# Optimization experiments

Hardware: AMD Instinct MI355X
Metric: run time of the kernel (lower is better)

The kernel has to match this reference:

```python
import jax, jax.numpy as jnp
import numpy as np

B, L, ENC, EMB, H, V = 64, 33, 512, 256, 512, 32000


def setup_inputs() -> dict:
    key = jax.random.key(0)
    ks = jax.random.split(key, 16)
    x = jax.random.normal(ks[0], (B, ENC), dtype=jnp.float32)
    padded_target = jax.random.randint(ks[1], (B, L), 0, V)
    target_lengths = jax.random.randint(ks[2], (B,), 2, L + 1)
    target_lengths = target_lengths.at[0].set(L)  # pin max length -> static step count
    s = 0.05
    return {
        "x": x,
        "padded_target": padded_target,
        "target_lengths": target_lengths,
        "embed": jax.random.normal(ks[3], (V, EMB), dtype=jnp.float32) * s,
        "W_h0": jax.random.normal(ks[4], (H, ENC), dtype=jnp.float32) * s,
        "b_h0": jnp.zeros((H,), jnp.float32),
        "W_c0": jax.random.normal(ks[5], (H, ENC), dtype=jnp.float32) * s,
        "b_c0": jnp.zeros((H,), jnp.float32),
        "W_ih": jax.random.normal(ks[6], (4 * H, ENC + EMB), dtype=jnp.float32) * s,
        "W_hh": jax.random.normal(ks[7], (4 * H, H), dtype=jnp.float32) * s,
        "b_ih": jnp.zeros((4 * H,), jnp.float32),
        "b_hh": jnp.zeros((4 * H,), jnp.float32),
        "W_out": jax.random.normal(ks[8], (V, H), dtype=jnp.float32) * s,
        "b_out": jnp.zeros((V,), jnp.float32),
    }


def reference(x, padded_target, target_lengths, embed, W_h0, b_h0, W_c0, b_c0,
              W_ih, W_hh, b_ih, b_hh, W_out, b_out):
    # sort by length, descending (packed-sequence ordering)
    sorted_indices = jnp.argsort(-target_lengths)
    x = x[sorted_indices]                      # [B, ENC]
    tgt = padded_target[sorted_indices]        # [B, L]
    lens = target_lengths[sorted_indices] - 1  # decode steps per row
    emb = embed[tgt]                           # [B, L, EMB]

    h = x @ W_h0.T + b_h0                      # context-initialized state
    c = x @ W_c0.T + b_c0
    T = padded_target.shape[1] - 1             # static max steps (max len pinned to L)

    def step(carry, inp):
        h, c = carry
        e_t, t = inp
        active = (lens > t)[:, None]           # rows still decoding (prefix, sorted)
        g = jnp.concatenate([x, e_t], axis=1) @ W_ih.T + b_ih + h @ W_hh.T + b_hh
        i, f, gg, o = jnp.split(g, 4, axis=1)  # torch LSTMCell gate order i,f,g,o
        c_new = jax.nn.sigmoid(f) * c + jax.nn.sigmoid(i) * jnp.tanh(gg)
        h_new = jax.nn.sigmoid(o) * jnp.tanh(c_new)
        h = jnp.where(active, h_new, h)        # inactive rows keep frozen state
        c = jnp.where(active, c_new, c)
        pred = jnp.where(active, h_new @ W_out.T + b_out, 0.0)  # dropout p=0
        return (h, c), pred

    (_, _), preds = jax.lax.scan(
        step, (h, c), (jnp.transpose(emb[:, :T], (1, 0, 2)), jnp.arange(T)))
    prediction = jnp.transpose(preds, (1, 0, 2))  # [B, T, V]
    return prediction, sorted_indices
```

## Files before the change

kernel.cpp:

```cpp
#include <hip/hip_runtime.h>

typedef __attribute__((ext_vector_type(8))) short short8;
typedef __attribute__((ext_vector_type(8))) unsigned short ushort8;
typedef __attribute__((ext_vector_type(4))) float f32x4;

#define DEV __device__ __forceinline__

DEV unsigned short f2bf(float f) {
  unsigned int u = __float_as_uint(f);
  u += 0x7fffu + ((u >> 16) & 1u);
  return (unsigned short)(u >> 16);
}
DEV float sigm(float x) { return 1.f / (1.f + __expf(-x)); }
DEV float tanh_(float x) { return 1.f - 2.f / (1.f + __expf(2.f * x)); }

typedef __attribute__((address_space(1))) const void* as1cv;
typedef __attribute__((address_space(3))) void* as3v;
DEV void gll16(const void* g, void* l) {
  __builtin_amdgcn_global_load_lds((as1cv)g, (as3v)l, 16, 0, 0);
}

__global__ void __launch_bounds__(256) k_sort(const float* __restrict__ x,
    const int* __restrict__ ptar, const int* __restrict__ tlen,
    int* __restrict__ sidx, int* __restrict__ lens, int* __restrict__ base,
    int* __restrict__ inv, int* __restrict__ Pw, int* __restrict__ tok,
    float* __restrict__ xs, float* __restrict__ tail) {
  __shared__ int ss[64], ls[64], bs[64];
  int tid = threadIdx.x;
  if (tid < 64) {
    int li = tlen[tid];
    int rank = 0;
    for (int j = 0; j < 64; ++j) {
      int lj = tlen[j];
      rank += (lj > li || (lj == li && j < tid)) ? 1 : 0;
    }
    ss[rank] = tid;
  }
  __syncthreads();
  if (tid < 64) {
    int src = ss[tid];
    sidx[tid] = src;
    int l = tlen[src] - 1;
    ls[tid] = l;
    lens[tid] = l;
    tail[tid] = (float)src;
  }
  __syncthreads();
  if (tid == 0) {
    int s = 0;
    for (int b = 0; b < 64; ++b) { bs[b] = s; base[b] = s; s += ls[b]; }
    Pw[0] = s;
  }
  __syncthreads();
  for (int idx = tid; idx < 2048; idx += 256) {
    int b = idx >> 5, t = idx & 31;
    if (t < ls[b]) inv[bs[b] + t] = idx;
  }
  for (int idx = tid; idx < 32 * 64; idx += 256) {
    int t = idx >> 6, b = idx & 63;
    tok[idx] = ptar[ss[b] * 33 + t];
  }
  for (int idx = tid; idx < 64 * 512; idx += 256) {
    int b = idx >> 9;
    xs[idx] = x[ss[b] * 512 + (idx & 511)];
  }
}

__global__ void __launch_bounds__(256) k_convmany(
    const float* __restrict__ W_h0, const float* __restrict__ W_c0,
    const float* __restrict__ W_ih, const float* __restrict__ W_hh,
    const float* __restrict__ xs,
    unsigned short* __restrict__ Wpro, unsigned short* __restrict__ Wihb2,
    unsigned short* __restrict__ Whb, unsigned short* __restrict__ xsb) {
  long long g = (long long)(blockIdx.x * 256 + threadIdx.x) * 8;
  const float* src;
  unsigned short* dst;
  if (g < 262144) {
    src = W_h0 + g; dst = Wpro + g;
  } else if (g < 524288) {
    long long l = g - 262144; src = W_c0 + l; dst = Wpro + 262144 + l;
  } else if (g < 1572864) {
    long long l = g - 524288;
    long long r = l >> 9, c = l & 511;
    src = W_ih + r * 768 + c; dst = Wpro + 524288 + l;
  } else if (g < 2097152) {
    long long l = g - 1572864;
    long long r = l >> 8, c = l & 255;
    src = W_ih + r * 768 + 512 + c; dst = Wihb2 + l;
  } else if (g < 3145728) {
    long long l = g - 2097152; src = W_hh + l; dst = Whb + l;
  } else {
    long long l = g - 3145728; src = xs + l; dst = xsb + l;
  }
  float4 v0 = *(const float4*)src, v1 = *(const float4*)(src + 4);
  ushort8 o;
  o[0] = f2bf(v0.x); o[1] = f2bf(v0.y); o[2] = f2bf(v0.z); o[3] = f2bf(v0.w);
  o[4] = f2bf(v1.x); o[5] = f2bf(v1.y); o[6] = f2bf(v1.z); o[7] = f2bf(v1.w);
  *(ushort8*)dst = o;
}

__global__ void __launch_bounds__(256) k_pro(const unsigned short* __restrict__ xsb,
    const unsigned short* __restrict__ Wpro, const float* __restrict__ b_h0,
    const float* __restrict__ b_c0, const float* __restrict__ b_ih,
    const float* __restrict__ b_hh, unsigned short* __restrict__ h0b,
    float* __restrict__ c, float* __restrict__ gx) {
  int tid = threadIdx.x, lane = tid & 63, w = tid >> 6;
  int n0 = blockIdx.x * 64 + w * 16;
  int lr = lane & 15, lk = lane >> 4;
  f32x4 acc[4];
#pragma unroll
  for (int i = 0; i < 4; ++i) acc[i] = (f32x4){0.f, 0.f, 0.f, 0.f};
  const unsigned short* B = Wpro + (size_t)(n0 + lr) * 512 + lk * 8;
  const unsigned short* A = xsb + (size_t)lr * 512 + lk * 8;
#pragma unroll
  for (int ks = 0; ks < 16; ++ks) {
    short8 bfr = *(const short8*)(B + ks * 32);
#pragma unroll
    for (int mi = 0; mi < 4; ++mi) {
      short8 af = *(const short8*)(A + mi * 16 * 512 + ks * 32);
      acc[mi] = __builtin_amdgcn_mfma_f32_16x16x32_bf16(af, bfr, acc[mi], 0, 0, 0);
    }
  }
  int n = n0 + lr;
#pragma unroll
  for (int mi = 0; mi < 4; ++mi)
#pragma unroll
    for (int r = 0; r < 4; ++r) {
      int b = mi * 16 + lk * 4 + r;
      float v = acc[mi][r];
      if (n < 512) {
        h0b[b * 512 + n] = f2bf(v + b_h0[n]);
      } else if (n < 1024) {
        int u = n - 512;
        c[b * 512 + u] = v + b_c0[u];
      } else {
        int j = n - 1024;
        gx[(size_t)b * 2048 + j] = v + b_ih[j] + b_hh[j];
      }
    }
}

__global__ void __launch_bounds__(256) k_emb(const int* __restrict__ tok,
    const float* __restrict__ embed, unsigned short* __restrict__ Eb) {
  int gid = blockIdx.x * 256 + threadIdx.x;
  int row = gid >> 5, c8 = (gid & 31) * 8;
  const float* src = embed + (size_t)tok[row] * 256 + c8;
  float4 v0 = *(const float4*)src, v1 = *(const float4*)(src + 4);
  ushort8 o;
  o[0] = f2bf(v0.x); o[1] = f2bf(v0.y); o[2] = f2bf(v0.z); o[3] = f2bf(v0.w);
  o[4] = f2bf(v1.x); o[5] = f2bf(v1.y); o[6] = f2bf(v1.z); o[7] = f2bf(v1.w);
  *(ushort8*)(Eb + (size_t)row * 256 + c8) = o;
}

__global__ void __launch_bounds__(256) k_ga2(const unsigned short* __restrict__ Eb,
    const unsigned short* __restrict__ Wb2, const float* __restrict__ gx,
    float* __restrict__ GA, const float* __restrict__ W_out,
    unsigned short* __restrict__ Wob) {
  int bid = blockIdx.x;
  int tid = threadIdx.x;
  if (bid >= 256) {
    long long basei = (long long)(bid - 256) * 65536;
#pragma unroll 4
    for (int it = 0; it < 32; ++it) {
      long long i = basei + (long long)it * 2048 + tid * 8;
      float4 v0 = *(const float4*)(W_out + i);
      float4 v1 = *(const float4*)(W_out + i + 4);
      ushort8 o;
      o[0] = f2bf(v0.x); o[1] = f2bf(v0.y); o[2] = f2bf(v0.z); o[3] = f2bf(v0.w);
      o[4] = f2bf(v1.x); o[5] = f2bf(v1.y); o[6] = f2bf(v1.z); o[7] = f2bf(v1.w);
      *(ushort8*)(Wob + i) = o;
    }
    return;
  }
  __shared__ alignas(16) char ldsbuf[32768];
  char* ldsA = ldsbuf;
  char* ldsB = ldsbuf + 16384;
  int mt = bid & 15, nt = bid >> 4;
  int m0 = mt * 128, n0 = nt * 128;
  int lane = tid & 63, w = tid >> 6;
  int wm = w >> 1, wn = w & 1;
  f32x4 acc[4][4];
#pragma unroll
  for (int a = 0; a < 4; ++a)
#pragma unroll
    for (int bq = 0; bq < 4; ++bq) acc[a][bq] = (f32x4){0.f, 0.f, 0.f, 0.f};
  const unsigned short* Arow = Eb + (size_t)m0 * 256;
  const unsigned short* Brow = Wb2 + (size_t)n0 * 256;
  for (int kt = 0; kt < 4; ++kt) {
    int k0 = kt * 64;
    if (kt) __syncthreads();
#pragma unroll
    for (int j = 0; j < 4; ++j) {
      int ci = j * 256 + w * 64 + lane;
      int r = ci >> 3;
      int clog = ((ci & 7) << 4) ^ ((r & 7) << 4);
      int ldst = (j * 256 + w * 64) * 16;
      gll16((const char*)(Arow + (size_t)r * 256 + k0) + clog, ldsA + ldst);
      gll16((const char*)(Brow + (size_t)r * 256 + k0) + clog, ldsB + ldst);
    }
    __syncthreads();
#pragma unroll
    for (int kk = 0; kk < 2; ++kk) {
      short8 af[4], bf[4];
      int cb = kk * 64 + (lane >> 4) * 16;
#pragma unroll
      for (int i = 0; i < 4; ++i) {
        int ar = wm * 64 + i * 16 + (lane & 15);
        af[i] = *(const short8*)(ldsA + ar * 128 + (cb ^ ((ar & 7) << 4)));
        int br = wn * 64 + i * 16 + (lane & 15);
        bf[i] = *(const short8*)(ldsB + br * 128 + (cb ^ ((br & 7) << 4)));
      }
#pragma unroll
      for (int mi = 0; mi < 4; ++mi)
#pragma unroll
        for (int ni = 0; ni < 4; ++ni)
          acc[mi][ni] = __builtin_amdgcn_mfma_f32_16x16x32_bf16(
              af[mi], bf[ni], acc[mi][ni], 0, 0, 0);
    }
  }
#pragma unroll
  for (int mi = 0; mi < 4; ++mi) {
    int mb = m0 + wm * 64 + mi * 16 + ((lane >> 4) << 2);
#pragma unroll
    for (int r = 0; r < 4; ++r) {
      int m = mb + r;
#pragma unroll
      for (int ni = 0; ni < 4; ++ni) {
        int j = n0 + wn * 64 + ni * 16 + (lane & 15);
        GA[(size_t)m * 2048 + j] = acc[mi][ni][r] + gx[(size_t)(m & 63) * 2048 + j];
      }
    }
  }
}

__global__ void __launch_bounds__(256) k_step3(
    const unsigned short* __restrict__ hin, unsigned short* __restrict__ hout,
    float* __restrict__ c, const float* __restrict__ GA,
    const unsigned short* __restrict__ Whb, const int* __restrict__ lens,
    const int* __restrict__ base, unsigned short* __restrict__ Hm, int t) {
  __shared__ float Gs[4][16][16];
  int tid = threadIdx.x, lane = tid & 63, g = tid >> 6;
  int lr = lane & 15, lk = lane >> 4;
  int mq = blockIdx.x & 3, ug = blockIdx.x >> 2;
  int r0 = mq * 16, u0 = ug * 16;

  const float* gab = GA + ((size_t)t * 64 + r0) * 2048 + g * 512 + u0 + lr;
  float gv[4];
#pragma unroll
  for (int r = 0; r < 4; ++r) gv[r] = gab[(size_t)(lk * 4 + r) * 2048];

  const unsigned short* Bp = Whb + (size_t)(g * 512 + u0 + lr) * 512 + lk * 8;
  const unsigned short* Ap = hin + (size_t)(r0 + lr) * 512 + lk * 8;
  f32x4 acc = (f32x4){0.f, 0.f, 0.f, 0.f};
#pragma unroll
  for (int ks = 0; ks < 16; ++ks) {
    short8 a0 = *(const short8*)(Ap + ks * 32);
    short8 b0 = *(const short8*)(Bp + ks * 32);
    acc = __builtin_amdgcn_mfma_f32_16x16x32_bf16(a0, b0, acc, 0, 0, 0);
  }
#pragma unroll
  for (int r = 0; r < 4; ++r) Gs[g][lk * 4 + r][lr] = acc[r] + gv[r];
  __syncthreads();

  int row = tid >> 4, uc = tid & 15;
  int b = r0 + row, u = u0 + uc;
  float fi = Gs[0][row][uc], ff = Gs[1][row][uc];
  float fg = Gs[2][row][uc], fo = Gs[3][row][uc];
  float cold = c[b * 512 + u];
  float cn = sigm(ff) * cold + sigm(fi) * tanh_(fg);
  float hn = sigm(fo) * tanh_(cn);
  bool act = lens[b] > t;
  if (act) c[b * 512 + u] = cn;
  unsigned short hbv = f2bf(hn);
  hout[b * 512 + u] = act ? hbv : hin[b * 512 + u];
  if (act) Hm[((size_t)(base[b] + t)) * 512 + u] = hbv;
}

__global__ void __launch_bounds__(256) k_zf(const int* __restrict__ lens,
    float* __restrict__ out) {
  int m = blockIdx.x;
  int b = m >> 5, t = m & 31;
  if (lens[b] > t) return;
  float4 z = {0.f, 0.f, 0.f, 0.f};
  float* row = out + (size_t)m * 32000;
  for (int i = threadIdx.x * 4; i < 32000; i += 1024)
    *(float4*)(row + i) = z;
}

__global__ void __launch_bounds__(512) k_gemm(const unsigned short* __restrict__ Hm,
    const unsigned short* __restrict__ Wb, const float* __restrict__ b_out,
    const int* __restrict__ inv, const int* __restrict__ Pw,
    float* __restrict__ out) {
  __shared__ alignas(16) char ldsbuf[49152];
  char* ldsA = ldsbuf;
  char* ldsB = ldsbuf + 16384;
  int P = Pw[0];
  int sb = (blockIdx.x & 7) * 250 + (blockIdx.x >> 3);
  int mt = sb % 16, nt = sb / 16;
  int m0 = mt * 128, n0 = nt * 256;
  if (m0 >= P) return;
  int tid = threadIdx.x, lane = tid & 63, w = tid >> 6;
  int wm = w >> 2, wn = w & 3;
  f32x4 acc[4][4];
#pragma unroll
  for (int a = 0; a < 4; ++a)
#pragma unroll
    for (int bq = 0; bq < 4; ++bq) acc[a][bq] = (f32x4){0.f, 0.f, 0.f, 0.f};
  const unsigned short* Arow = Hm + (size_t)m0 * 512;
  const unsigned short* Brow = Wb + (size_t)n0 * 512;
  for (int kt = 0; kt < 8; ++kt) {
    int k0 = kt * 64;
    if (kt) __syncthreads();
#pragma unroll
    for (int j = 0; j < 2; ++j) {
      int ci = j * 512 + tid;
      int r = ci >> 3;
      int clog = ((ci & 7) << 4) ^ ((r & 7) << 4);
      gll16((const char*)(Arow + (size_t)r * 512 + k0) + clog, ldsA + ci * 16);
    }
#pragma unroll
    for (int j = 0; j < 4; ++j) {
      int ci = j * 512 + tid;
      int r = ci >> 3;
      int clog = ((ci & 7) << 4) ^ ((r & 7) << 4);
      gll16((const char*)(Brow + (size_t)r * 512 + k0) + clog, ldsB + ci * 16);
    }
    __syncthreads();
#pragma unroll
    for (int kk = 0; kk < 2; ++kk) {
      short8 af[4], bf[4];
      int cb = kk * 64 + (lane >> 4) * 16;
#pragma unroll
      for (int i = 0; i < 4; ++i) {
        int ar = wm * 64 + i * 16 + (lane & 15);
        af[i] = *(const short8*)(ldsA + ar * 128 + (cb ^ ((ar & 7) << 4)));
        int br = wn * 64 + i * 16 + (lane & 15);
        bf[i] = *(const short8*)(ldsB + br * 128 + (cb ^ ((br & 7) << 4)));
      }
#pragma unroll
      for (int mi = 0; mi < 4; ++mi)
#pragma unroll
        for (int ni = 0; ni < 4; ++ni)
          acc[mi][ni] = __builtin_amdgcn_mfma_f32_16x16x32_bf16(
              af[mi], bf[ni], acc[mi][ni], 0, 0, 0);
    }
  }
#pragma unroll
  for (int mi = 0; mi < 4; ++mi) {
    int pb = m0 + wm * 64 + mi * 16 + ((lane >> 4) << 2);
#pragma unroll
    for (int r = 0; r < 4; ++r) {
      int p = pb + r;
      if (p >= P) continue;
      size_t orow = (size_t)inv[p] * 32000;
#pragma unroll
      for (int ni = 0; ni < 4; ++ni) {
        int n = n0 + wn * 64 + ni * 16 + (lane & 15);
        out[orow + n] = acc[mi][ni][r] + b_out[n];
      }
    }
  }
}

extern "C" void kernel_launch(void* const* d_in, const int* in_sizes, int n_in,
                              void* d_out, int out_size, void* d_ws, size_t ws_size,
                              hipStream_t stream) {
  const float* x     = (const float*)d_in[0];
  const int*   ptar  = (const int*)d_in[1];
  const int*   tlen  = (const int*)d_in[2];
  const float* embed = (const float*)d_in[3];
  const float* W_h0  = (const float*)d_in[4];
  const float* b_h0  = (const float*)d_in[5];
  const float* W_c0  = (const float*)d_in[6];
  const float* b_c0  = (const float*)d_in[7];
  const float* W_ih  = (const float*)d_in[8];
  const float* W_hh  = (const float*)d_in[9];
  const float* b_ih  = (const float*)d_in[10];
  const float* b_hh  = (const float*)d_in[11];
  const float* W_out = (const float*)d_in[12];
  const float* b_out = (const float*)d_in[13];
  float* out = (float*)d_out;

  char* ws = (char*)d_ws;
  size_t off = 0;
  auto alloc = [&](size_t bytes) {
    void* p = ws + off;
    off += (bytes + 255) & ~(size_t)255;
    return p;
  };
  unsigned short* Wob = (unsigned short*)alloc(32000ull * 512 * 2);
  unsigned short* Hm  = (unsigned short*)alloc(2048ull * 512 * 2);
  float* xs   = (float*)alloc(64 * 512 * 4);
  unsigned short* h0b = (unsigned short*)alloc(64 * 512 * 2);
  unsigned short* h1b = (unsigned short*)alloc(64 * 512 * 2);
  float* cbuf = (float*)alloc(64 * 512 * 4);
  float* gx   = (float*)alloc(64 * 2048 * 4);
  int* sidx = (int*)alloc(64 * 4);
  int* lens = (int*)alloc(64 * 4);
  int* base = (int*)alloc(64 * 4);
  int* inv  = (int*)alloc(2048 * 4);
  int* Pw   = (int*)alloc(4);
  int* tok  = (int*)alloc(2048 * 4);

  float* GA = out;
  unsigned short* Wpro  = (unsigned short*)(out + 4194304);
  unsigned short* Wihb2 = (unsigned short*)(out + 4980736);
  unsigned short* Whb   = (unsigned short*)(out + 5242880);
  unsigned short* Eb    = (unsigned short*)(out + 5767168);
  unsigned short* xsb   = (unsigned short*)(out + 6029312);
  float* tail = out + 65536000;

  k_sort<<<1, 256, 0, stream>>>(x, ptar, tlen, sidx, lens, base, inv, Pw, tok,
                                xs, tail);
  k_convmany<<<1552, 256, 0, stream>>>(W_h0, W_c0, W_ih, W_hh, xs,
                                       Wpro, Wihb2, Whb, xsb);
  k_pro<<<48, 256, 0, stream>>>(xsb, Wpro, b_h0, b_c0, b_ih, b_hh, h0b, cbuf, gx);
  k_emb<<<256, 256, 0, stream>>>(tok, embed, Eb);
  k_ga2<<<506, 256, 0, stream>>>(Eb, Wihb2, gx, GA, W_out, Wob);

  unsigned short* hb[2] = {h0b, h1b};
  for (int t = 0; t < 32; ++t)
    k_step3<<<128, 256, 0, stream>>>(hb[t & 1], hb[(t + 1) & 1], cbuf, GA, Whb,
                                     lens, base, Hm, t);

  k_zf<<<2048, 256, 0, stream>>>(lens, out);
  k_gemm<<<2000, 512, 0, stream>>>(Hm, Wob, b_out, inv, Pw, out);
  (void)in_sizes; (void)n_in; (void)out_size; (void)ws_size;
}
```

Measured before the change: 362.4 us.

## Fuse prep kernels and overlap W_out conversion with recurrent steps

```diff
diff --git a/kernel.cpp b/kernel.cpp
--- a/kernel.cpp
+++ b/kernel.cpp
@@ -20,13 +20,43 @@
   __builtin_amdgcn_global_load_lds((as1cv)g, (as3v)l, 16, 0, 0);
 }
 
-__global__ void __launch_bounds__(256) k_sort(const float* __restrict__ x,
+__global__ void __launch_bounds__(256) k_pre(const float* __restrict__ x,
     const int* __restrict__ ptar, const int* __restrict__ tlen,
+    const float* __restrict__ W_h0, const float* __restrict__ W_c0,
+    const float* __restrict__ W_ih, const float* __restrict__ W_hh,
     int* __restrict__ sidx, int* __restrict__ lens, int* __restrict__ base,
     int* __restrict__ inv, int* __restrict__ Pw, int* __restrict__ tok,
-    float* __restrict__ xs, float* __restrict__ tail) {
+    unsigned short* __restrict__ xsb, float* __restrict__ tail,
+    unsigned short* __restrict__ Wpro, unsigned short* __restrict__ Wihb2,
+    unsigned short* __restrict__ Whb) {
+  int bid = blockIdx.x, tid = threadIdx.x;
+  if (bid > 0) {
+    long long g = (long long)(bid - 1) * 2048 + tid * 8;
+    const float* src;
+    unsigned short* dst;
+    if (g < 262144) {
+      src = W_h0 + g; dst = Wpro + g;
+    } else if (g < 524288) {
+      long long l = g - 262144; src = W_c0 + l; dst = Wpro + 262144 + l;
+    } else if (g < 1572864) {
+      long long l = g - 524288;
+      long long r = l >> 9, c = l & 511;
+      src = W_ih + r * 768 + c; dst = Wpro + 524288 + l;
+    } else if (g < 2097152) {
+      long long l = g - 1572864;
+      long long r = l >> 8, c = l & 255;
+      src = W_ih + r * 768 + 512 + c; dst = Wihb2 + l;
+    } else {
+      long long l = g - 2097152; src = W_hh + l; dst = Whb + l;
+    }
+    float4 v0 = *(const float4*)src, v1 = *(const float4*)(src + 4);
+    ushort8 o;
+    o[0] = f2bf(v0.x); o[1] = f2bf(v0.y); o[2] = f2bf(v0.z); o[3] = f2bf(v0.w);
+    o[4] = f2bf(v1.x); o[5] = f2bf(v1.y); o[6] = f2bf(v1.z); o[7] = f2bf(v1.w);
+    *(ushort8*)dst = o;
+    return;
+  }
   __shared__ int ss[64], ls[64], bs[64];
-  int tid = threadIdx.x;
   if (tid < 64) {
     int li = tlen[tid];
     int rank = 0;
@@ -62,50 +92,31 @@
   }
   for (int idx = tid; idx < 64 * 512; idx += 256) {
     int b = idx >> 9;
-    xs[idx] = x[ss[b] * 512 + (idx & 511)];
-  }
-}
-
-__global__ void __launch_bounds__(256) k_convmany(
-    const float* __restrict__ W_h0, const float* __restrict__ W_c0,
-    const float* __restrict__ W_ih, const float* __restrict__ W_hh,
-    const float* __restrict__ xs,
-    unsigned short* __restrict__ Wpro, unsigned short* __restrict__ Wihb2,
-    unsigned short* __restrict__ Whb, unsigned short* __restrict__ xsb) {
-  long long g = (long long)(blockIdx.x * 256 + threadIdx.x) * 8;
-  const float* src;
-  unsigned short* dst;
-  if (g < 262144) {
-    src = W_h0 + g; dst = Wpro + g;
-  } else if (g < 524288) {
-    long long l = g - 262144; src = W_c0 + l; dst = Wpro + 262144 + l;
-  } else if (g < 1572864) {
-    long long l = g - 524288;
-    long long r = l >> 9, c = l & 511;
-    src = W_ih + r * 768 + c; dst = Wpro + 524288 + l;
-  } else if (g < 2097152) {
-    long long l = g - 1572864;
-    long long r = l >> 8, c = l & 255;
-    src = W_ih + r * 768 + 512 + c; dst = Wihb2 + l;
-  } else if (g < 3145728) {
-    long long l = g - 2097152; src = W_hh + l; dst = Whb + l;
-  } else {
-    long long l = g - 3145728; src = xs + l; dst = xsb + l;
-  }
-  float4 v0 = *(const float4*)src, v1 = *(const float4*)(src + 4);
-  ushort8 o;
-  o[0] = f2bf(v0.x); o[1] = f2bf(v0.y); o[2] = f2bf(v0.z); o[3] = f2bf(v0.w);
-  o[4] = f2bf(v1.x); o[5] = f2bf(v1.y); o[6] = f2bf(v1.z); o[7] = f2bf(v1.w);
-  *(ushort8*)dst = o;
-}
-
-__global__ void __launch_bounds__(256) k_pro(const unsigned short* __restrict__ xsb,
+    xsb[idx] = f2bf(x[ss[b] * 512 + (idx & 511)]);
+  }
+}
+
+__global__ void __launch_bounds__(256) k_mid(const unsigned short* __restrict__ xsb,
     const unsigned short* __restrict__ Wpro, const float* __restrict__ b_h0,
     const float* __restrict__ b_c0, const float* __restrict__ b_ih,
     const float* __restrict__ b_hh, unsigned short* __restrict__ h0b,
-    float* __restrict__ c, float* __restrict__ gx) {
-  int tid = threadIdx.x, lane = tid & 63, w = tid >> 6;
-  int n0 = blockIdx.x * 64 + w * 16;
+    float* __restrict__ c, float* __restrict__ gx,
+    const int* __restrict__ tok, const float* __restrict__ embed,
+    unsigned short* __restrict__ Eb) {
+  int bid = blockIdx.x, tid = threadIdx.x;
+  if (bid >= 48) {
+    int gid = (bid - 48) * 256 + tid;
+    int row = gid >> 5, c8 = (gid & 31) * 8;
+    const float* src = embed + (size_t)tok[row] * 256 + c8;
+    float4 v0 = *(const float4*)src, v1 = *(const float4*)(src + 4);
+    ushort8 o;
+    o[0] = f2bf(v0.x); o[1] = f2bf(v0.y); o[2] = f2bf(v0.z); o[3] = f2bf(v0.w);
+    o[4] = f2bf(v1.x); o[5] = f2bf(v1.y); o[6] = f2bf(v1.z); o[7] = f2bf(v1.w);
+    *(ushort8*)(Eb + (size_t)row * 256 + c8) = o;
+    return;
+  }
+  int lane = tid & 63, w = tid >> 6;
+  int n0 = bid * 64 + w * 16;
   int lr = lane & 15, lk = lane >> 4;
   f32x4 acc[4];
 #pragma unroll
@@ -140,41 +151,13 @@
     }
 }
 
-__global__ void __launch_bounds__(256) k_emb(const int* __restrict__ tok,
-    const float* __restrict__ embed, unsigned short* __restrict__ Eb) {
-  int gid = blockIdx.x * 256 + threadIdx.x;
-  int row = gid >> 5, c8 = (gid & 31) * 8;
-  const float* src = embed + (size_t)tok[row] * 256 + c8;
-  float4 v0 = *(const float4*)src, v1 = *(const float4*)(src + 4);
-  ushort8 o;
-  o[0] = f2bf(v0.x); o[1] = f2bf(v0.y); o[2] = f2bf(v0.z); o[3] = f2bf(v0.w);
-  o[4] = f2bf(v1.x); o[5] = f2bf(v1.y); o[6] = f2bf(v1.z); o[7] = f2bf(v1.w);
-  *(ushort8*)(Eb + (size_t)row * 256 + c8) = o;
-}
-
 __global__ void __launch_bounds__(256) k_ga2(const unsigned short* __restrict__ Eb,
     const unsigned short* __restrict__ Wb2, const float* __restrict__ gx,
-    float* __restrict__ GA, const float* __restrict__ W_out,
-    unsigned short* __restrict__ Wob) {
-  int bid = blockIdx.x;
-  int tid = threadIdx.x;
-  if (bid >= 256) {
-    long long basei = (long long)(bid - 256) * 65536;
-#pragma unroll 4
-    for (int it = 0; it < 32; ++it) {
-      long long i = basei + (long long)it * 2048 + tid * 8;
-      float4 v0 = *(const float4*)(W_out + i);
-      float4 v1 = *(const float4*)(W_out + i + 4);
-      ushort8 o;
-      o[0] = f2bf(v0.x); o[1] = f2bf(v0.y); o[2] = f2bf(v0.z); o[3] = f2bf(v0.w);
-      o[4] = f2bf(v1.x); o[5] = f2bf(v1.y); o[6] = f2bf(v1.z); o[7] = f2bf(v1.w);
-      *(ushort8*)(Wob + i) = o;
-    }
-    return;
-  }
+    float* __restrict__ GA) {
   __shared__ alignas(16) char ldsbuf[32768];
   char* ldsA = ldsbuf;
   char* ldsB = ldsbuf + 16384;
+  int bid = blockIdx.x, tid = threadIdx.x;
   int mt = bid & 15, nt = bid >> 4;
   int m0 = mt * 128, n0 = nt * 128;
   int lane = tid & 63, w = tid >> 6;
@@ -237,11 +220,26 @@
     const unsigned short* __restrict__ hin, unsigned short* __restrict__ hout,
     float* __restrict__ c, const float* __restrict__ GA,
     const unsigned short* __restrict__ Whb, const int* __restrict__ lens,
-    const int* __restrict__ base, unsigned short* __restrict__ Hm, int t) {
+    const int* __restrict__ base, unsigned short* __restrict__ Hm,
+    const float* __restrict__ W_out, unsigned short* __restrict__ Wob, int t) {
+  int tid = threadIdx.x, bid = blockIdx.x;
+  if (bid >= 128) {
+    long long s0 = (long long)t * 512000 + (long long)(bid - 128) * 64000;
+    long long s1 = s0 + 64000;
+    for (long long i = s0 + tid * 8; i < s1; i += 2048) {
+      float4 v0 = *(const float4*)(W_out + i);
+      float4 v1 = *(const float4*)(W_out + i + 4);
+      ushort8 o;
+      o[0] = f2bf(v0.x); o[1] = f2bf(v0.y); o[2] = f2bf(v0.z); o[3] = f2bf(v0.w);
+      o[4] = f2bf(v1.x); o[5] = f2bf(v1.y); o[6] = f2bf(v1.z); o[7] = f2bf(v1.w);
+      *(ushort8*)(Wob + i) = o;
+    }
+    return;
+  }
   __shared__ float Gs[4][16][16];
-  int tid = threadIdx.x, lane = tid & 63, g = tid >> 6;
+  int lane = tid & 63, g = tid >> 6;
   int lr = lane & 15, lk = lane >> 4;
-  int mq = blockIdx.x & 3, ug = blockIdx.x >> 2;
+  int mq = bid & 3, ug = bid >> 2;
   int r0 = mq * 16, u0 = ug * 16;
 
   const float* gab = GA + ((size_t)t * 64 + r0) * 2048 + g * 512 + u0 + lr;
@@ -276,31 +274,34 @@
   if (act) Hm[((size_t)(base[b] + t)) * 512 + u] = hbv;
 }
 
-__global__ void __launch_bounds__(256) k_zf(const int* __restrict__ lens,
-    float* __restrict__ out) {
-  int m = blockIdx.x;
-  int b = m >> 5, t = m & 31;
-  if (lens[b] > t) return;
-  float4 z = {0.f, 0.f, 0.f, 0.f};
-  float* row = out + (size_t)m * 32000;
-  for (int i = threadIdx.x * 4; i < 32000; i += 1024)
-    *(float4*)(row + i) = z;
-}
-
-__global__ void __launch_bounds__(512) k_gemm(const unsigned short* __restrict__ Hm,
+__global__ void __launch_bounds__(256) k_gemm(const unsigned short* __restrict__ Hm,
     const unsigned short* __restrict__ Wb, const float* __restrict__ b_out,
     const int* __restrict__ inv, const int* __restrict__ Pw,
-    float* __restrict__ out) {
-  __shared__ alignas(16) char ldsbuf[49152];
+    const int* __restrict__ lens, float* __restrict__ out) {
+  int bid = blockIdx.x, tid = threadIdx.x;
+  if (bid >= 4000) {
+    int idx = bid - 4000;
+    float4 z = {0.f, 0.f, 0.f, 0.f};
+#pragma unroll
+    for (int k = 0; k < 4; ++k) {
+      int m = idx * 4 + k;
+      int b = m >> 5, t = m & 31;
+      if (lens[b] > t) continue;
+      float* row = out + (size_t)m * 32000;
+      for (int i = tid * 4; i < 32000; i += 1024) *(float4*)(row + i) = z;
+    }
+    return;
+  }
+  __shared__ alignas(16) char ldsbuf[32768];
   char* ldsA = ldsbuf;
   char* ldsB = ldsbuf + 16384;
   int P = Pw[0];
-  int sb = (blockIdx.x & 7) * 250 + (blockIdx.x >> 3);
-  int mt = sb % 16, nt = sb / 16;
-  int m0 = mt * 128, n0 = nt * 256;
+  int sb = (bid & 7) * 500 + (bid >> 3);
+  int mt = sb & 15, nt = sb >> 4;
+  int m0 = mt * 128, n0 = nt * 128;
   if (m0 >= P) return;
-  int tid = threadIdx.x, lane = tid & 63, w = tid >> 6;
-  int wm = w >> 2, wn = w & 3;
+  int lane = tid & 63, w = tid >> 6;
+  int wm = w >> 1, wn = w & 1;
   f32x4 acc[4][4];
 #pragma unroll
   for (int a = 0; a < 4; ++a)
@@ -312,18 +313,13 @@
     int k0 = kt * 64;
     if (kt) __syncthreads();
 #pragma unroll
-    for (int j = 0; j < 2; ++j) {
-      int ci = j * 512 + tid;
+    for (int j = 0; j < 4; ++j) {
+      int ci = j * 256 + w * 64 + lane;
       int r = ci >> 3;
       int clog = ((ci & 7) << 4) ^ ((r & 7) << 4);
-      gll16((const char*)(Arow + (size_t)r * 512 + k0) + clog, ldsA + ci * 16);
-    }
-#pragma unroll
-    for (int j = 0; j < 4; ++j) {
-      int ci = j * 512 + tid;
-      int r = ci >> 3;
-      int clog = ((ci & 7) << 4) ^ ((r & 7) << 4);
-      gll16((const char*)(Brow + (size_t)r * 512 + k0) + clog, ldsB + ci * 16);
+      int ldst = (j * 256 + w * 64) * 16;
+      gll16((const char*)(Arow + (size_t)r * 512 + k0) + clog, ldsA + ldst);
+      gll16((const char*)(Brow + (size_t)r * 512 + k0) + clog, ldsB + ldst);
     }
     __syncthreads();
 #pragma unroll
@@ -390,7 +386,6 @@
   };
   unsigned short* Wob = (unsigned short*)alloc(32000ull * 512 * 2);
   unsigned short* Hm  = (unsigned short*)alloc(2048ull * 512 * 2);
-  float* xs   = (float*)alloc(64 * 512 * 4);
   unsigned short* h0b = (unsigned short*)alloc(64 * 512 * 2);
   unsigned short* h1b = (unsigned short*)alloc(64 * 512 * 2);
   float* cbuf = (float*)alloc(64 * 512 * 4);
@@ -410,20 +405,18 @@
   unsigned short* xsb   = (unsigned short*)(out + 6029312);
   float* tail = out + 65536000;
 
-  k_sort<<<1, 256, 0, stream>>>(x, ptar, tlen, sidx, lens, base, inv, Pw, tok,
-                                xs, tail);
-  k_convmany<<<1552, 256, 0, stream>>>(W_h0, W_c0, W_ih, W_hh, xs,
-                                       Wpro, Wihb2, Whb, xsb);
-  k_pro<<<48, 256, 0, stream>>>(xsb, Wpro, b_h0, b_c0, b_ih, b_hh, h0b, cbuf, gx);
-  k_emb<<<256, 256, 0, stream>>>(tok, embed, Eb);
-  k_ga2<<<506, 256, 0, stream>>>(Eb, Wihb2, gx, GA, W_out, Wob);
+  k_pre<<<1537, 256, 0, stream>>>(x, ptar, tlen, W_h0, W_c0, W_ih, W_hh,
+                                  sidx, lens, base, inv, Pw, tok, xsb, tail,
+                                  Wpro, Wihb2, Whb);
+  k_mid<<<304, 256, 0, stream>>>(xsb, Wpro, b_h0, b_c0, b_ih, b_hh, h0b, cbuf,
+                                 gx, tok, embed, Eb);
+  k_ga2<<<256, 256, 0, stream>>>(Eb, Wihb2, gx, GA);
 
   unsigned short* hb[2] = {h0b, h1b};
   for (int t = 0; t < 32; ++t)
-    k_step3<<<128, 256, 0, stream>>>(hb[t & 1], hb[(t + 1) & 1], cbuf, GA, Whb,
-                                     lens, base, Hm, t);
-
-  k_zf<<<2048, 256, 0, stream>>>(lens, out);
-  k_gemm<<<2000, 512, 0, stream>>>(Hm, Wob, b_out, inv, Pw, out);
+    k_step3<<<136, 256, 0, stream>>>(hb[t & 1], hb[(t + 1) & 1], cbuf, GA, Whb,
+                                     lens, base, Hm, W_out, Wob, t);
+
+  k_gemm<<<4512, 256, 0, stream>>>(Hm, Wob, b_out, inv, Pw, lens, out);
   (void)in_sizes; (void)n_in; (void)out_size; (void)ws_size;
 }
```

After: 735.1 us. 103% more time.
